# Performance work log

Hardware: AMD Instinct MI355X
Metric: run time of the kernel (lower is better)

The kernel has to match this reference:

```python
import jax, jax.numpy as jnp
import numpy as np

D_MODEL = 1024
NUM_HEADS = 16
DEPTH = D_MODEL // NUM_HEADS
B, S = 4, 2048


def setup_inputs() -> dict:
    key = jax.random.key(0)
    ks = jax.random.split(key, 12)
    s = 1.0 / np.sqrt(D_MODEL)
    return {
        "q": jax.random.normal(ks[0], (B, S, D_MODEL), jnp.float32),
        "k": jax.random.normal(ks[1], (B, S, D_MODEL), jnp.float32),
        "v": jax.random.normal(ks[2], (B, S, D_MODEL), jnp.float32),
        "mask": jax.random.randint(ks[3], (B, S), 0, 2, jnp.int32),
        "wq_w": jax.random.uniform(ks[4], (D_MODEL, D_MODEL), jnp.float32, -s, s),
        "wq_b": jnp.zeros((D_MODEL,), jnp.float32),
        "wk_w": jax.random.uniform(ks[5], (D_MODEL, D_MODEL), jnp.float32, -s, s),
        "wk_b": jnp.zeros((D_MODEL,), jnp.float32),
        "wv_w": jax.random.uniform(ks[6], (D_MODEL, D_MODEL), jnp.float32, -s, s),
        "wv_b": jnp.zeros((D_MODEL,), jnp.float32),
        "wo_w": jax.random.uniform(ks[7], (D_MODEL, D_MODEL), jnp.float32, -s, s),
        "wo_b": jnp.zeros((D_MODEL,), jnp.float32),
    }


def _split_heads(x):
    # [B, S, D] -> [B, H, S, depth]
    b, s, _ = x.shape
    return x.reshape(b, s, NUM_HEADS, DEPTH).transpose(0, 2, 1, 3)


def reference(q, k, v, mask, wq_w, wq_b, wk_w, wk_b, wv_w, wv_b, wo_w, wo_b):
    qh = _split_heads(q @ wq_w.T + wq_b)
    kh = _split_heads(k @ wk_w.T + wk_b)
    vh = _split_heads(v @ wv_w.T + wv_b)
    # [B, H, Sq, Sk]
    logits = jnp.einsum("bhqd,bhkd->bhqk", qh, kh) / jnp.sqrt(
        jnp.asarray(DEPTH, jnp.float32))
    # 2D mask -> [B, 1, 1, Sk], masked_fill where mask == 0
    m = mask[:, None, None, :]
    logits = jnp.where(m == 0, jnp.asarray(-1e9, logits.dtype), logits)
    attn = jax.nn.softmax(logits, axis=-1)
    out = jnp.einsum("bhqk,bhkd->bhqd", attn, vh)
    out = out.transpose(0, 2, 1, 3).reshape(q.shape[0], -1, D_MODEL)
    return out @ wo_w.T + wo_b
```

## Files before the change

### kernel.cpp

```cpp
#include <hip/hip_runtime.h>
#include <hip/hip_bf16.h>
#include <stdint.h>

typedef __bf16 bf16_t;
typedef __bf16 bf16x8 __attribute__((ext_vector_type(8)));
typedef __bf16 bf16x2 __attribute__((ext_vector_type(2)));
typedef float  f32x4  __attribute__((ext_vector_type(4)));
typedef float  f32x16 __attribute__((ext_vector_type(16)));
typedef unsigned int u32;
typedef u32 u32x4 __attribute__((ext_vector_type(4)));

#define D_MODEL 1024
#define NHEAD   16
#define DEPTH   64
#define BATCH   4
#define SEQ     2048
#define MROWS   (BATCH*SEQ)

#define SC 0.18033688011112042f

__device__ __forceinline__ void gload16(const void* g, void* l) {
    __builtin_amdgcn_global_load_lds(
        (__attribute__((address_space(1))) void*)(uintptr_t)g,
        (__attribute__((address_space(3))) void*)l,
        16, 0, 0);
}

__device__ __forceinline__ u32 pk2(float a, float b) {
    bf16x2 t; t[0] = (bf16_t)a; t[1] = (bf16_t)b;
    return __builtin_bit_cast(u32, t);
}

__global__ __launch_bounds__(256) void cvt_kernel(const float* __restrict__ src,
                                                  bf16_t* __restrict__ dst, int n8) {
    int i = blockIdx.x * 256 + threadIdx.x;
    if (i >= n8) return;
    const float4* s4 = (const float4*)src;
    float4 a = s4[2*(size_t)i], b = s4[2*(size_t)i + 1];
    bf16x8 o;
    o[0] = (bf16_t)a.x; o[1] = (bf16_t)a.y; o[2] = (bf16_t)a.z; o[3] = (bf16_t)a.w;
    o[4] = (bf16_t)b.x; o[5] = (bf16_t)b.y; o[6] = (bf16_t)b.z; o[7] = (bf16_t)b.w;
    *(bf16x8*)(dst + 8*(size_t)i) = o;
}

__global__ __launch_bounds__(256) void cvtw_kernel(const float* __restrict__ s0, bf16_t* __restrict__ d0,
                                                   const float* __restrict__ s1, bf16_t* __restrict__ d1,
                                                   const float* __restrict__ s2, bf16_t* __restrict__ d2,
                                                   const float* __restrict__ s3, bf16_t* __restrict__ d3,
                                                   int n8) {
    int i = blockIdx.x * 256 + threadIdx.x;
    if (i >= n8) return;
    const float* src; bf16_t* dst;
    switch (blockIdx.y) {
        case 0: src = s0; dst = d0; break;
        case 1: src = s1; dst = d1; break;
        case 2: src = s2; dst = d2; break;
        default: src = s3; dst = d3; break;
    }
    const float4* s4 = (const float4*)src;
    float4 a = s4[2*(size_t)i], b = s4[2*(size_t)i + 1];
    bf16x8 o;
    o[0] = (bf16_t)a.x; o[1] = (bf16_t)a.y; o[2] = (bf16_t)a.z; o[3] = (bf16_t)a.w;
    o[4] = (bf16_t)b.x; o[5] = (bf16_t)b.y; o[6] = (bf16_t)b.z; o[7] = (bf16_t)b.w;
    *(bf16x8*)(dst + 8*(size_t)i) = o;
}

template<int MODE>
__global__ __launch_bounds__(256) void gemm_bt(const bf16_t* __restrict__ A,
                                               const bf16_t* __restrict__ Bw,
                                               const float* __restrict__ bias,
                                               bf16_t* __restrict__ Cb,
                                               float* __restrict__ Cf,
                                               int M, int N, int K, float scale) {
    __shared__ bf16_t Smem[2*128*64];
    bf16_t* As = Smem;
    bf16_t* Bs = Smem + 128*64;
    const int tid  = threadIdx.x;
    const int wave = tid >> 6, lane = tid & 63;
    const int lr = lane & 15, lk = (lane >> 4) * 8;
    const int bm = blockIdx.x * 128, bn = blockIdx.y * 128;
    const int wr = (wave >> 1) * 64, wc = (wave & 1) * 64;

    f32x4 acc[4][4] = {};

    for (int kt = 0; kt < K; kt += 64) {
#pragma unroll
        for (int p = 0; p < 4; ++p) {
            int chunk = p*256 + tid;
            int r  = chunk >> 3;
            int cs = ((chunk & 7) ^ (r & 7)) * 8;
            gload16(A  + (size_t)(bm + r)*K + kt + cs, As + (size_t)(p*256 + wave*64)*8);
            gload16(Bw + (size_t)(bn + r)*K + kt + cs, Bs + (size_t)(p*256 + wave*64)*8);
        }
        __syncthreads();
        const char* AsB = (const char*)As;
        const char* BsB = (const char*)Bs;
#pragma unroll
        for (int ks = 0; ks < 2; ++ks) {
            int kb = (ks*32 + lk) * 2;
            bf16x8 af[4], bfv[4];
#pragma unroll
            for (int mi = 0; mi < 4; ++mi) {
                int row = wr + mi*16 + lr;
                af[mi] = *(const bf16x8*)(AsB + ((row*128 + kb) ^ ((row & 7) << 4)));
            }
#pragma unroll
            for (int ni = 0; ni < 4; ++ni) {
                int row = wc + ni*16 + lr;
                bfv[ni] = *(const bf16x8*)(BsB + ((row*128 + kb) ^ ((row & 7) << 4)));
            }
            __builtin_amdgcn_s_setprio(1);
#pragma unroll
            for (int mi = 0; mi < 4; ++mi)
#pragma unroll
                for (int ni = 0; ni < 4; ++ni)
                    acc[mi][ni] = __builtin_amdgcn_mfma_f32_16x16x32_bf16(
                        af[mi], bfv[ni], acc[mi][ni], 0, 0, 0);
            __builtin_amdgcn_s_setprio(0);
        }
        __syncthreads();
    }

    if (MODE != 2) {
#pragma unroll
        for (int ni = 0; ni < 4; ++ni) {
            int col = bn + wc + ni*16 + lr;
            float bv = bias[col];
#pragma unroll
            for (int mi = 0; mi < 4; ++mi) {
#pragma unroll
                for (int j = 0; j < 4; ++j) {
                    int row = bm + wr + mi*16 + (lane >> 4)*4 + j;
                    float vv = (acc[mi][ni][j] + bv) * scale;
                    if (MODE == 1) Cb[(size_t)row*N + col] = (bf16_t)vv;
                    else           Cf[(size_t)row*N + col] = vv;
                }
            }
        }
    } else {
        char* TB = (char*)Smem;
#pragma unroll
        for (int ni = 0; ni < 4; ++ni) {
            int col = wc + ni*16 + lr;
            int swz = (col & 7) << 4;
            float bv = bias[bn + col];
#pragma unroll
            for (int mi = 0; mi < 4; ++mi)
#pragma unroll
                for (int j = 0; j < 4; ++j) {
                    int row = wr + mi*16 + (lane >> 4)*4 + j;
                    int sp  = (row & ~12) | ((row & 4) << 1) | ((row & 8) >> 1);
                    float vv = (acc[mi][ni][j] + bv) * scale;
                    *(bf16_t*)(TB + ((col*256 + sp*2) ^ swz)) = (bf16_t)vv;
                }
        }
        __syncthreads();
        const int b = bm >> 11, sl = bm & 2047;
#pragma unroll
        for (int p = 0; p < 8; ++p) {
            int id = p*256 + tid;
            int col = id >> 4, sg = id & 15;
            bf16x8 v8 = *(const bf16x8*)(TB + ((col*256 + sg*16) ^ ((col & 7) << 4)));
            int gc = bn + col;
            int bh = b*16 + (gc >> 6), d = gc & 63;
            *(bf16x8*)&Cb[((size_t)bh*DEPTH + d)*SEQ + sl + sg*8] = v8;
        }
    }
}

__global__ __launch_bounds__(256, 3) void attn_kernel(const bf16_t* __restrict__ Qp,
                                                      const bf16_t* __restrict__ Kp,
                                                      const bf16_t* __restrict__ Vt,
                                                      const int* __restrict__ mask,
                                                      bf16_t* __restrict__ AO) {
    __shared__ bf16_t Ks[3][64*64];
    __shared__ bf16_t Vs[3][64*64];
    __shared__ bf16_t mbias[SEQ];

    const int tid  = threadIdx.x;
    const int wave = tid >> 6, lane = tid & 63;
    const int lr5 = lane & 31;
    const int hi  = lane >> 5;

    const int flat = blockIdx.x + 16*blockIdx.y + 256*blockIdx.z;
    const int xcd = flat & 7, slot = flat >> 3;
    const int bh = xcd + 8*(slot >> 4);
    const int b = bh >> 4, h = bh & 15;
    const int q0 = (slot & 15) * 128;

    const int qw = q0 + wave*32;
    const size_t base  = (size_t)b * SEQ * D_MODEL + (size_t)h * DEPTH;
    const size_t vbase = (size_t)bh * DEPTH * SEQ;

    bf16x8 qf[4];
#pragma unroll
    for (int dc = 0; dc < 4; ++dc)
        qf[dc] = *(const bf16x8*)&Qp[base + (size_t)(qw + lr5)*D_MODEL + dc*16 + hi*8];

    u32x4 onew = {};
    onew[0] = hi ? 0u : 0x3F80u;
    const bf16x8 qone = __builtin_bit_cast(bf16x8, onew);

    u32x4 lonesw = {};
    if (lr5 == 0) { lonesw[0] = 0x3F803F80u; lonesw[1] = 0x3F803F80u;
                    lonesw[2] = 0x3F803F80u; lonesw[3] = 0x3F803F80u; }
    const bf16x8 onesA = __builtin_bit_cast(bf16x8, lonesw);

    {
        const int4* mp = (const int4*)&mask[(size_t)b*SEQ + tid*8];
        int4 m0 = mp[0], m1 = mp[1];
        bf16x8 mm;
        mm[0] = (m0.x == 0) ? (bf16_t)(-1e30f) : (bf16_t)0.0f;
        mm[1] = (m0.y == 0) ? (bf16_t)(-1e30f) : (bf16_t)0.0f;
        mm[2] = (m0.z == 0) ? (bf16_t)(-1e30f) : (bf16_t)0.0f;
        mm[3] = (m0.w == 0) ? (bf16_t)(-1e30f) : (bf16_t)0.0f;
        mm[4] = (m1.x == 0) ? (bf16_t)(-1e30f) : (bf16_t)0.0f;
        mm[5] = (m1.y == 0) ? (bf16_t)(-1e30f) : (bf16_t)0.0f;
        mm[6] = (m1.z == 0) ? (bf16_t)(-1e30f) : (bf16_t)0.0f;
        mm[7] = (m1.w == 0) ? (bf16_t)(-1e30f) : (bf16_t)0.0f;
        *(bf16x8*)&mbias[tid*8] = mm;
    }

    auto stage = [&](int t, int buf) {
#pragma unroll
        for (int p = 0; p < 2; ++p) {
            int chunk = p*256 + tid; int r = chunk >> 3;
            int cs = ((chunk & 7) ^ (r & 7)) * 8;
            gload16(Kp + base + (size_t)(t*64 + r)*D_MODEL + cs,
                    (bf16_t*)Ks[buf] + (size_t)chunk*8);
            gload16(Vt + vbase + (size_t)r*SEQ + t*64 + cs,
                    (bf16_t*)Vs[buf] + (size_t)chunk*8);
        }
    };

    f32x16 o0 = {}, o1 = {};
    f32x16 l_acc = {};

    stage(0, 0); stage(1, 1); stage(2, 2);
    asm volatile("s_waitcnt vmcnt(8) lgkmcnt(0)");
    __builtin_amdgcn_s_barrier();

    int cb = 0;
    for (int t = 0; t < SEQ/64; ++t) {
        u32 mw0 = (u32)__builtin_bit_cast(unsigned short, mbias[t*64 + lr5]);
        u32 mw1 = (u32)__builtin_bit_cast(unsigned short, mbias[t*64 + 32 + lr5]);
        if (hi) { mw0 = 0; mw1 = 0; }
        u32x4 mv0 = {}, mv1 = {};
        mv0[0] = mw0; mv1[0] = mw1;
        bf16x8 afm0 = __builtin_bit_cast(bf16x8, mv0);
        bf16x8 afm1 = __builtin_bit_cast(bf16x8, mv1);

        const char* KsB = (const char*)Ks[cb];
        const f32x16 zz = {};
        f32x16 s0, s1;
        __builtin_amdgcn_s_setprio(1);
        s0 = __builtin_amdgcn_mfma_f32_32x32x16_bf16(afm0, qone, zz, 0, 0, 0);
        s1 = __builtin_amdgcn_mfma_f32_32x32x16_bf16(afm1, qone, zz, 0, 0, 0);
#pragma unroll
        for (int dc = 0; dc < 4; ++dc) {
            int colb = dc*32 + hi*16;
            int row0 = lr5, row1 = 32 + lr5;
            bf16x8 kf0 = *(const bf16x8*)(KsB + ((row0*128 + colb) ^ ((row0 & 7) << 4)));
            bf16x8 kf1 = *(const bf16x8*)(KsB + ((row1*128 + colb) ^ ((row1 & 7) << 4)));
            s0 = __builtin_amdgcn_mfma_f32_32x32x16_bf16(kf0, qf[dc], s0, 0, 0, 0);
            s1 = __builtin_amdgcn_mfma_f32_32x32x16_bf16(kf1, qf[dc], s1, 0, 0, 0);
        }
        __builtin_amdgcn_s_setprio(0);

        const char* VsB = (const char*)Vs[cb];
#pragma unroll
        for (int kt = 0; kt < 2; ++kt) {
            const f32x16& sh = kt ? s1 : s0;
            float pv[16];
#pragma unroll
            for (int r = 0; r < 16; ++r) pv[r] = __builtin_exp2f(sh[r]);
#pragma unroll
            for (int c = 0; c < 2; ++c) {
                u32x4 fwv;
#pragma unroll
                for (int i = 0; i < 4; ++i)
                    fwv[i] = pk2(pv[c*8 + 2*i], pv[c*8 + 2*i + 1]);
                bf16x8 pfrag = __builtin_bit_cast(bf16x8, fwv);
                int colb = kt*64 + c*32 + hi*16;
                int row0 = lr5, row1 = 32 + lr5;
                bf16x8 vf0 = *(const bf16x8*)(VsB + ((row0*128 + colb) ^ ((row0 & 7) << 4)));
                bf16x8 vf1 = *(const bf16x8*)(VsB + ((row1*128 + colb) ^ ((row1 & 7) << 4)));
                __builtin_amdgcn_s_setprio(1);
                o0 = __builtin_amdgcn_mfma_f32_32x32x16_bf16(vf0, pfrag, o0, 0, 0, 0);
                o1 = __builtin_amdgcn_mfma_f32_32x32x16_bf16(vf1, pfrag, o1, 0, 0, 0);
                l_acc = __builtin_amdgcn_mfma_f32_32x32x16_bf16(onesA, pfrag, l_acc, 0, 0, 0);
                __builtin_amdgcn_s_setprio(0);
            }
        }

        asm volatile("s_waitcnt vmcnt(4) lgkmcnt(0)");
        __builtin_amdgcn_s_barrier();
        if (t + 3 < SEQ/64) stage(t + 3, cb);
        ++cb; if (cb == 3) cb = 0;
    }

    float l_tot = l_acc[0] + __shfl_xor(l_acc[0], 32);
    float inv = 1.f / l_tot;
    char* TrB = (char*)Ks;
    const int qloc = wave*32 + lr5;
#pragma unroll
    for (int mt = 0; mt < 2; ++mt)
#pragma unroll
        for (int r = 0; r < 16; ++r) {
            int d = mt*32 + (r & 3) + 8*(r >> 2) + 4*hi;
            float val = (mt ? o1[r] : o0[r]) * inv;
            *(bf16_t*)(TrB + (qloc*128 + ((d*2) ^ ((qloc & 7) << 4)))) = (bf16_t)val;
        }
    __syncthreads();
#pragma unroll
    for (int p = 0; p < 4; ++p) {
        int id = p*256 + tid;
        int row = id >> 3, g = id & 7;
        bf16x8 v8 = *(const bf16x8*)(TrB + (row*128 + ((g*16) ^ ((row & 7) << 4))));
        *(bf16x8*)&AO[base + (size_t)(q0 + row)*D_MODEL + g*8] = v8;
    }
}

extern "C" void kernel_launch(void* const* d_in, const int* in_sizes, int n_in,
                              void* d_out, int out_size, void* d_ws, size_t ws_size,
                              hipStream_t stream) {
    (void)in_sizes; (void)n_in; (void)out_size; (void)ws_size;
    const float* q    = (const float*)d_in[0];
    const float* k    = (const float*)d_in[1];
    const float* v    = (const float*)d_in[2];
    const int*   mask = (const int*)d_in[3];
    const float* wq_w = (const float*)d_in[4];
    const float* wq_b = (const float*)d_in[5];
    const float* wk_w = (const float*)d_in[6];
    const float* wk_b = (const float*)d_in[7];
    const float* wv_w = (const float*)d_in[8];
    const float* wv_b = (const float*)d_in[9];
    const float* wo_w = (const float*)d_in[10];
    const float* wo_b = (const float*)d_in[11];
    float* out = (float*)d_out;

    const size_t ACT = (size_t)MROWS * D_MODEL;
    const size_t WSZ = (size_t)D_MODEL * D_MODEL;
    bf16_t* Xb = (bf16_t*)d_ws;
    bf16_t* Qp = Xb + ACT;
    bf16_t* Kp = Qp + ACT;
    bf16_t* Vt = Kp + ACT;
    bf16_t* Wq = Vt + ACT;
    bf16_t* Wk = Wq + WSZ;
    bf16_t* Wv = Wk + WSZ;
    bf16_t* Wo = Wv + WSZ;
    bf16_t* AO = Xb;

    const int wn8 = (int)(WSZ/8), an8 = (int)(ACT/8);
    cvtw_kernel<<<dim3(wn8/256, 4), dim3(256), 0, stream>>>(wq_w, Wq, wk_w, Wk, wv_w, Wv, wo_w, Wo, wn8);

    dim3 ggrid(MROWS/128, D_MODEL/128);
    cvt_kernel<<<dim3(an8/256), dim3(256), 0, stream>>>(q, Xb, an8);
    gemm_bt<1><<<ggrid, dim3(256), 0, stream>>>(Xb, Wq, wq_b, Qp, nullptr, MROWS, D_MODEL, D_MODEL, SC);
    cvt_kernel<<<dim3(an8/256), dim3(256), 0, stream>>>(k, Xb, an8);
    gemm_bt<1><<<ggrid, dim3(256), 0, stream>>>(Xb, Wk, wk_b, Kp, nullptr, MROWS, D_MODEL, D_MODEL, 1.f);
    cvt_kernel<<<dim3(an8/256), dim3(256), 0, stream>>>(v, Xb, an8);
    gemm_bt<2><<<ggrid, dim3(256), 0, stream>>>(Xb, Wv, wv_b, Vt, nullptr, MROWS, D_MODEL, D_MODEL, 1.f);

    attn_kernel<<<dim3(SEQ/128, NHEAD, BATCH), dim3(256), 0, stream>>>(Qp, Kp, Vt, mask, AO);

    gemm_bt<0><<<ggrid, dim3(256), 0, stream>>>(AO, Wo, wo_b, nullptr, out, MROWS, D_MODEL, D_MODEL, 1.f);
}
```

Baseline: 243.1 us.

## Batch activation conversions, remap GEMM tile order, sum softmax denominator in VALU

The three activation fp32-to-bf16 conversions now run as one launch over four buffers, and the workspace is reassigned so projections no longer reuse a single staging buffer. GEMM blocks are flattened so that consecutive blocks cover the 8 N-tiles of the same M row-panel, which should improve reuse of A in L2. In attention, the row-sum MFMA against a ones matrix is replaced by scalar accumulation of the exp values followed by a cross-half shuffle. This removes one MFMA per P·V step, at the cost of extra VALU adds.

```diff
diff --git a/kernel.cpp b/kernel.cpp
--- a/kernel.cpp
+++ b/kernel.cpp
@@ -31,10 +31,18 @@
     return __builtin_bit_cast(u32, t);
 }
 
-__global__ __launch_bounds__(256) void cvt_kernel(const float* __restrict__ src,
-                                                  bf16_t* __restrict__ dst, int n8) {
+__global__ __launch_bounds__(256) void cvt3_kernel(const float* __restrict__ s0, bf16_t* __restrict__ d0,
+                                                   const float* __restrict__ s1, bf16_t* __restrict__ d1,
+                                                   const float* __restrict__ s2, bf16_t* __restrict__ d2,
+                                                   int n8) {
     int i = blockIdx.x * 256 + threadIdx.x;
     if (i >= n8) return;
+    const float* src; bf16_t* dst;
+    switch (blockIdx.y) {
+        case 0: src = s0; dst = d0; break;
+        case 1: src = s1; dst = d1; break;
+        default: src = s2; dst = d2; break;
+    }
     const float4* s4 = (const float4*)src;
     float4 a = s4[2*(size_t)i], b = s4[2*(size_t)i + 1];
     bf16x8 o;
@@ -78,7 +86,7 @@
     const int tid  = threadIdx.x;
     const int wave = tid >> 6, lane = tid & 63;
     const int lr = lane & 15, lk = (lane >> 4) * 8;
-    const int bm = blockIdx.x * 128, bn = blockIdx.y * 128;
+    const int bm = (blockIdx.x >> 3) * 128, bn = (blockIdx.x & 7) * 128;
     const int wr = (wave >> 1) * 64, wc = (wave & 1) * 64;
 
     f32x4 acc[4][4] = {};
@@ -200,11 +208,6 @@
     u32x4 onew = {};
     onew[0] = hi ? 0u : 0x3F80u;
     const bf16x8 qone = __builtin_bit_cast(bf16x8, onew);
-
-    u32x4 lonesw = {};
-    if (lr5 == 0) { lonesw[0] = 0x3F803F80u; lonesw[1] = 0x3F803F80u;
-                    lonesw[2] = 0x3F803F80u; lonesw[3] = 0x3F803F80u; }
-    const bf16x8 onesA = __builtin_bit_cast(bf16x8, lonesw);
 
     {
         const int4* mp = (const int4*)&mask[(size_t)b*SEQ + tid*8];
@@ -234,7 +237,7 @@
     };
 
     f32x16 o0 = {}, o1 = {};
-    f32x16 l_acc = {};
+    float l_run = 0.f;
 
     stage(0, 0); stage(1, 1); stage(2, 2);
     asm volatile("s_waitcnt vmcnt(8) lgkmcnt(0)");
@@ -274,6 +277,12 @@
             float pv[16];
 #pragma unroll
             for (int r = 0; r < 16; ++r) pv[r] = __builtin_exp2f(sh[r]);
+            float su0 = 0.f, su1 = 0.f, su2 = 0.f, su3 = 0.f;
+#pragma unroll
+            for (int r = 0; r < 16; r += 4) {
+                su0 += pv[r]; su1 += pv[r+1]; su2 += pv[r+2]; su3 += pv[r+3];
+            }
+            l_run += (su0 + su1) + (su2 + su3);
 #pragma unroll
             for (int c = 0; c < 2; ++c) {
                 u32x4 fwv;
@@ -288,7 +297,6 @@
                 __builtin_amdgcn_s_setprio(1);
                 o0 = __builtin_amdgcn_mfma_f32_32x32x16_bf16(vf0, pfrag, o0, 0, 0, 0);
                 o1 = __builtin_amdgcn_mfma_f32_32x32x16_bf16(vf1, pfrag, o1, 0, 0, 0);
-                l_acc = __builtin_amdgcn_mfma_f32_32x32x16_bf16(onesA, pfrag, l_acc, 0, 0, 0);
                 __builtin_amdgcn_s_setprio(0);
             }
         }
@@ -299,7 +307,7 @@
         ++cb; if (cb == 3) cb = 0;
     }
 
-    float l_tot = l_acc[0] + __shfl_xor(l_acc[0], 32);
+    float l_tot = l_run + __shfl_xor(l_run, 32);
     float inv = 1.f / l_tot;
     char* TrB = (char*)Ks;
     const int qloc = wave*32 + lr5;
@@ -341,28 +349,25 @@
 
     const size_t ACT = (size_t)MROWS * D_MODEL;
     const size_t WSZ = (size_t)D_MODEL * D_MODEL;
-    bf16_t* Xb = (bf16_t*)d_ws;
-    bf16_t* Qp = Xb + ACT;
-    bf16_t* Kp = Qp + ACT;
-    bf16_t* Vt = Kp + ACT;
-    bf16_t* Wq = Vt + ACT;
+    bf16_t* B0 = (bf16_t*)d_ws;
+    bf16_t* B1 = B0 + ACT;
+    bf16_t* B2 = B1 + ACT;
+    bf16_t* B3 = B2 + ACT;
+    bf16_t* Wq = B3 + ACT;
     bf16_t* Wk = Wq + WSZ;
     bf16_t* Wv = Wk + WSZ;
     bf16_t* Wo = Wv + WSZ;
-    bf16_t* AO = Xb;
 
     const int wn8 = (int)(WSZ/8), an8 = (int)(ACT/8);
     cvtw_kernel<<<dim3(wn8/256, 4), dim3(256), 0, stream>>>(wq_w, Wq, wk_w, Wk, wv_w, Wv, wo_w, Wo, wn8);
-
-    dim3 ggrid(MROWS/128, D_MODEL/128);
-    cvt_kernel<<<dim3(an8/256), dim3(256), 0, stream>>>(q, Xb, an8);
-    gemm_bt<1><<<ggrid, dim3(256), 0, stream>>>(Xb, Wq, wq_b, Qp, nullptr, MROWS, D_MODEL, D_MODEL, SC);
-    cvt_kernel<<<dim3(an8/256), dim3(256), 0, stream>>>(k, Xb, an8);
-    gemm_bt<1><<<ggrid, dim3(256), 0, stream>>>(Xb, Wk, wk_b, Kp, nullptr, MROWS, D_MODEL, D_MODEL, 1.f);
-    cvt_kernel<<<dim3(an8/256), dim3(256), 0, stream>>>(v, Xb, an8);
-    gemm_bt<2><<<ggrid, dim3(256), 0, stream>>>(Xb, Wv, wv_b, Vt, nullptr, MROWS, D_MODEL, D_MODEL, 1.f);
-
-    attn_kernel<<<dim3(SEQ/128, NHEAD, BATCH), dim3(256), 0, stream>>>(Qp, Kp, Vt, mask, AO);
-
-    gemm_bt<0><<<ggrid, dim3(256), 0, stream>>>(AO, Wo, wo_b, nullptr, out, MROWS, D_MODEL, D_MODEL, 1.f);
-}
+    cvt3_kernel<<<dim3(an8/256, 3), dim3(256), 0, stream>>>(q, B0, k, B1, v, B2, an8);
+
+    const int ggrid = (MROWS/128) * (D_MODEL/128);
+    gemm_bt<1><<<ggrid, dim3(256), 0, stream>>>(B0, Wq, wq_b, B3, nullptr, MROWS, D_MODEL, D_MODEL, SC);
+    gemm_bt<1><<<ggrid, dim3(256), 0, stream>>>(B1, Wk, wk_b, B0, nullptr, MROWS, D_MODEL, D_MODEL, 1.f);
+    gemm_bt<2><<<ggrid, dim3(256), 0, stream>>>(B2, Wv, wv_b, B1, nullptr, MROWS, D_MODEL, D_MODEL, 1.f);
+
+    attn_kernel<<<dim3(SEQ/128, NHEAD, BATCH), dim3(256), 0, stream>>>(B3, B0, B1, mask, B2);
+
+    gemm_bt<0><<<ggrid, dim3(256), 0, stream>>>(B2, Wo, wo_b, nullptr, out, MROWS, D_MODEL, D_MODEL, 1.f);
+}
```

New measurement: 231.2 us. -4.9%, faster.
